# Performance work log

Hardware: AMD Instinct MI355X
Metric: run time of the kernel (lower is better)

## Reference

```python
import jax, jax.numpy as jnp
import numpy as np

N, F, E = 1024, 32, 20


def setup_inputs() -> dict:
    key = jax.random.key(0)
    ks = jax.random.split(key, 18)
    f32 = jnp.float32
    nrm = lambda k, shape, s=1.0: (jax.random.normal(k, shape, f32) * s)
    scalar = nrm(ks[0], (N, 1, F))
    vector = nrm(ks[1], (N, 3, F))
    expansion = nrm(ks[2], (N, N, E))
    d = nrm(ks[3], (N, N, 3))
    direction = d / (jnp.linalg.norm(d, axis=-1, keepdims=True) + 1e-6)
    mask = (jax.random.uniform(ks[4], (N, N, 1)) < 0.9).astype(f32)
    w = 0.1  # weight scale
    return {
        "scalar": scalar, "vector": vector, "expansion": expansion,
        "direction": direction, "mask": mask,
        # message.msg_left: Linear(F,F) -> SiLU -> Linear(F,3F)
        "mL_w1": nrm(ks[5], (F, F), w), "mL_b1": jnp.zeros((F,), f32),
        "mL_w2": nrm(ks[6], (F, 3 * F), w), "mL_b2": jnp.zeros((3 * F,), f32),
        # message.msg_right: Linear(E, 3F)
        "mR_w": nrm(ks[7], (E, 3 * F), w), "mR_b": jnp.zeros((3 * F,), f32),
        # update.upd_right: Linear(2F,F) -> SiLU -> Linear(F,3F)
        "uR_w1": nrm(ks[8], (2 * F, F), w), "uR_b1": jnp.zeros((F,), f32),
        "uR_w2": nrm(ks[9], (F, 3 * F), w), "uR_b2": jnp.zeros((3 * F,), f32),
        # update.U / update.V: Linear(F,F,bias=False)
        "U_w": nrm(ks[10], (F, F), w),
        "V_w": nrm(ks[11], (F, F), w),
    }


def _message(s, v, expansion, direction, mask,
             mL_w1, mL_b1, mL_w2, mL_b2, mR_w, mR_b):
    # msg_left(s): [N,1,F] -> [N,1,3F]
    left = jax.nn.silu(s @ mL_w1 + mL_b1) @ mL_w2 + mL_b2
    # msg_right(expansion): [N,N,E] -> [N,N,3F] -> [N,N,1,3F]
    right = (expansion @ mR_w + mR_b)[..., None, :]
    prod = left * right                      # [N,N,1,3F]
    a, b, c = jnp.split(prod, 3, axis=-1)    # each [N,N,1,F]
    mask_ = mask[..., None]                  # [N,N,1,1]
    delta_s = jnp.sum(mask_ * b, axis=-3)    # [N,1,F]
    dv = v * a + direction[..., None] * c    # [N,N,3,F]
    delta_v = jnp.sum(mask_ * dv, axis=-3)   # [N,3,F]
    return delta_s, delta_v


def _update(scalar, vector, uR_w1, uR_b1, uR_w2, uR_b2, U_w, V_w):
    left = vector @ U_w                      # [N,3,F]
    right = vector @ V_w                     # [N,3,F]
    right_norm = jnp.linalg.norm(right, axis=-2, keepdims=True)   # [N,1,F]
    feats = jnp.concatenate((scalar, right_norm), axis=-1)        # [N,1,2F]
    feats = jax.nn.silu(feats @ uR_w1 + uR_b1) @ uR_w2 + uR_b2    # [N,1,3F]
    a, b, c = jnp.split(feats, 3, axis=-1)
    delta_v = a * left                                            # [N,3,F]
    inner = jnp.sum(left * right, axis=-2, keepdims=True)         # [N,1,F]
    delta_s = inner * b + c
    return delta_s, delta_v


def reference(scalar, vector, expansion, direction, mask,
              mL_w1, mL_b1, mL_w2, mL_b2, mR_w, mR_b,
              uR_w1, uR_b1, uR_w2, uR_b2, U_w, V_w):
    ds, dv = _message(scalar, vector, expansion, direction, mask,
                      mL_w1, mL_b1, mL_w2, mL_b2, mR_w, mR_b)
    scalar = scalar + ds
    vector = vector + dv
    ds, dv = _update(scalar, vector, uR_w1, uR_b1, uR_w2, uR_b2, U_w, V_w)
    return scalar + ds, vector + dv
```

## Files before the change

### kernel.cpp

```cpp
#include <hip/hip_runtime.h>
#include <hip/hip_bf16.h>
#include <math.h>

#define NN 1024

typedef __attribute__((ext_vector_type(8))) short v8s;
typedef __attribute__((ext_vector_type(4))) float v4f;

#define MFMA(a, b, c) __builtin_amdgcn_mfma_f32_16x16x32_bf16((a), (b), (c), 0, 0, 0)

static __device__ __forceinline__ float silu_f(float x) {
    return x / (1.0f + __expf(-x));
}
static __device__ __forceinline__ unsigned short f2bf(float x) {
    __hip_bfloat16 h = __float2bfloat16(x);
    unsigned short u; __builtin_memcpy(&u, &h, 2); return u;
}
static __device__ __forceinline__ unsigned pack2bf(float lo, float hi) {
    __hip_bfloat162 h = __float22bfloat162_rn(make_float2(lo, hi));
    unsigned u; __builtin_memcpy(&u, &h, 4); return u;
}

extern "C" __global__ __launch_bounds__(128)
void node_kernel(const float* __restrict__ scalar,
                 const float* __restrict__ vector,
                 const float* __restrict__ mL_w1, const float* __restrict__ mL_b1,
                 const float* __restrict__ mL_w2, const float* __restrict__ mL_b2,
                 unsigned short* __restrict__ RT)
{
    const int j = blockIdx.x;
    const int t = threadIdx.x;
    __shared__ float ss[32], sh[32], sleft[96];

    if (t < 32) ss[t] = scalar[j * 32 + t];
    __syncthreads();
    if (t < 32) {
        float a = mL_b1[t];
        #pragma unroll
        for (int k = 0; k < 32; k++) a = fmaf(ss[k], mL_w1[k * 32 + t], a);
        sh[t] = silu_f(a);
    }
    __syncthreads();
    if (t < 96) {
        float a = mL_b2[t];
        #pragma unroll
        for (int k = 0; k < 32; k++) a = fmaf(sh[k], mL_w2[k * 96 + t], a);
        sleft[t] = a;
    }
    __syncthreads();
    for (int n = t; n < 160; n += 128) {
        float val;
        if (n < 32)        val = sleft[32 + n];
        else if (n < 128)  val = vector[j * 96 + (n - 32)] * sleft[(n - 32) & 31];
        else               val = sleft[64 + (n - 128)];
        RT[(size_t)n * NN + j] = f2bf(val);
    }
}

extern "C" __global__ __launch_bounds__(128, 3)
void edge_mfma_kernel(const float* __restrict__ scalar,
                      const float* __restrict__ vector,
                      const float* __restrict__ expansion,
                      const float* __restrict__ direction,
                      const float* __restrict__ mask,
                      const float* __restrict__ mR_w, const float* __restrict__ mR_b,
                      const float* __restrict__ uR_w1, const float* __restrict__ uR_b1,
                      const float* __restrict__ uR_w2, const float* __restrict__ uR_b2,
                      const float* __restrict__ U_w,  const float* __restrict__ V_w,
                      const unsigned short* __restrict__ RT,
                      float* __restrict__ out)
{
    const int i = blockIdx.x;
    const int t = threadIdx.x;
    const int wave = t >> 6;
    const int lane = t & 63;
    const int lrow = lane & 15;
    const int quad = lane >> 4;

    __shared__ __align__(16) char smem[24576];
    unsigned short* L1 = (unsigned short*)smem;
    unsigned short* L2 = L1 + 32 * 72;
    float* T1 = (float*)smem;
    float* T2 = T1 + 32 * 128;
    __shared__ float snew[32], vnew[96], lUs[96], rVs[96], rnorm[32], h2s[32], f2s[96];

    v4f acc[12];
    #pragma unroll
    for (int q = 0; q < 12; ++q) acc[q] = (v4f){0.f, 0.f, 0.f, 0.f};

    const int jp = t >> 2;
    const int g  = t & 3;
    const int jl = jp * 2;

    for (int chunk = 0; chunk < 16; ++chunk) {
        const int j0 = chunk * 64;
        {
            const size_t jg = (size_t)i * NN + j0 + jl;
            const float4* ep = (const float4*)(expansion + jg * 20);
            const float m0 = mask[jg], m1 = mask[jg + 1];
            float w0, w1;
            unsigned short *Lp, *Lx;
            if (g == 0) {
                w0 = m0; w1 = m1;
                Lp = L1; Lx = L1 + 20 * 72;
            } else {
                const int d = g - 1;
                w0 = m0 * direction[jg * 3 + d];
                w1 = m1 * direction[(jg + 1) * 3 + d];
                Lp = L2 + d * 20 * 72; Lx = L2 + (60 + d) * 72;
            }
            #pragma unroll
            for (int q = 0; q < 5; ++q) {
                const float4 a = ep[q];
                const float4 b = ep[5 + q];
                *(unsigned*)(Lp + (4 * q + 0) * 72 + jl) = pack2bf(w0 * a.x, w1 * b.x);
                *(unsigned*)(Lp + (4 * q + 1) * 72 + jl) = pack2bf(w0 * a.y, w1 * b.y);
                *(unsigned*)(Lp + (4 * q + 2) * 72 + jl) = pack2bf(w0 * a.z, w1 * b.z);
                *(unsigned*)(Lp + (4 * q + 3) * 72 + jl) = pack2bf(w0 * a.w, w1 * b.w);
            }
            *(unsigned*)(Lx + jl) = pack2bf(w0, w1);
        }
        __syncthreads();
        #pragma unroll
        for (int s = 0; s < 2; ++s) {
            const int koff = s * 32 + quad * 8;
            const v8s a0 = *(const v8s*)(L1 + (lrow) * 72 + koff);
            const v8s a1 = *(const v8s*)(L1 + (16 + lrow) * 72 + koff);
            const unsigned short* Bp = RT + (size_t)lrow * NN + j0 + koff;
            if (wave == 0) {
                #pragma unroll
                for (int nt = 0; nt < 6; ++nt) {
                    const v8s b = *(const v8s*)(Bp + (size_t)nt * 16 * NN);
                    acc[nt]     = MFMA(a0, b, acc[nt]);
                    acc[6 + nt] = MFMA(a1, b, acc[6 + nt]);
                }
            } else {
                const v8s b6 = *(const v8s*)(Bp + (size_t)6 * 16 * NN);
                const v8s b7 = *(const v8s*)(Bp + (size_t)7 * 16 * NN);
                acc[0] = MFMA(a0, b6, acc[0]);
                acc[1] = MFMA(a0, b7, acc[1]);
                acc[2] = MFMA(a1, b6, acc[2]);
                acc[3] = MFMA(a1, b7, acc[3]);
                const v8s d0 = *(const v8s*)(Bp + (size_t)8 * 16 * NN);
                const v8s d1 = *(const v8s*)(Bp + (size_t)9 * 16 * NN);
                #pragma unroll
                for (int mt = 0; mt < 4; ++mt) {
                    const v8s c = *(const v8s*)(L2 + (mt * 16 + lrow) * 72 + koff);
                    acc[4 + mt * 2]     = MFMA(c, d0, acc[4 + mt * 2]);
                    acc[4 + mt * 2 + 1] = MFMA(c, d1, acc[4 + mt * 2 + 1]);
                }
            }
        }
        __syncthreads();
    }

    if (wave == 0) {
        #pragma unroll
        for (int mt = 0; mt < 2; ++mt)
        #pragma unroll
        for (int nt = 0; nt < 6; ++nt) {
            const v4f a = acc[mt * 6 + nt];
            #pragma unroll
            for (int r = 0; r < 4; ++r)
                T1[(mt * 16 + quad * 4 + r) * 128 + nt * 16 + lrow] = a[r];
        }
    } else {
        #pragma unroll
        for (int mt = 0; mt < 2; ++mt)
        #pragma unroll
        for (int nb = 0; nb < 2; ++nb) {
            const v4f a = acc[mt * 2 + nb];
            #pragma unroll
            for (int r = 0; r < 4; ++r)
                T1[(mt * 16 + quad * 4 + r) * 128 + (6 + nb) * 16 + lrow] = a[r];
        }
        #pragma unroll
        for (int mt = 0; mt < 4; ++mt)
        #pragma unroll
        for (int nb = 0; nb < 2; ++nb) {
            const v4f a = acc[4 + mt * 2 + nb];
            #pragma unroll
            for (int r = 0; r < 4; ++r)
                T2[(mt * 16 + quad * 4 + r) * 32 + nb * 16 + lrow] = a[r];
        }
    }
    __syncthreads();

    if (t < 32) {
        const int f = t;
        float a = mR_b[32 + f] * T1[20 * 128 + f];
        #pragma unroll
        for (int e = 0; e < 20; ++e) a = fmaf(mR_w[e * 96 + 32 + f], T1[e * 128 + f], a);
        snew[f] = scalar[i * 32 + f] + a;
    } else if (t < 128) {
        const int q = t - 32, d = q >> 5, f = q & 31;
        const int col = 32 + q;
        float a = mR_b[f] * T1[20 * 128 + col];
        #pragma unroll
        for (int e = 0; e < 20; ++e) a = fmaf(mR_w[e * 96 + f], T1[e * 128 + col], a);
        float c = mR_b[64 + f] * T2[(60 + d) * 32 + f];
        #pragma unroll
        for (int e = 0; e < 20; ++e) c = fmaf(mR_w[e * 96 + 64 + f], T2[(d * 20 + e) * 32 + f], c);
        vnew[q] = vector[i * 96 + q] + a + c;
    }
    __syncthreads();

    if (t < 96) {
        const int d = t >> 5, f = t & 31;
        float au = 0.f, av = 0.f;
        #pragma unroll
        for (int k = 0; k < 32; ++k) {
            const float vv = vnew[d * 32 + k];
            au = fmaf(vv, U_w[k * 32 + f], au);
            av = fmaf(vv, V_w[k * 32 + f], av);
        }
        lUs[t] = au; rVs[t] = av;
    }
    __syncthreads();
    if (t < 32)
        rnorm[t] = sqrtf(rVs[t] * rVs[t] + rVs[32 + t] * rVs[32 + t] + rVs[64 + t] * rVs[64 + t]);
    __syncthreads();
    if (t < 32) {
        float a = uR_b1[t];
        #pragma unroll
        for (int k = 0; k < 32; ++k) a = fmaf(snew[k], uR_w1[k * 32 + t], a);
        #pragma unroll
        for (int k = 0; k < 32; ++k) a = fmaf(rnorm[k], uR_w1[(32 + k) * 32 + t], a);
        h2s[t] = silu_f(a);
    }
    __syncthreads();
    if (t < 96) {
        float a = uR_b2[t];
        #pragma unroll
        for (int k = 0; k < 32; ++k) a = fmaf(h2s[k], uR_w2[k * 96 + t], a);
        f2s[t] = a;
    }
    __syncthreads();
    if (t < 32) {
        const float inner = lUs[t] * rVs[t] + lUs[32 + t] * rVs[32 + t] + lUs[64 + t] * rVs[64 + t];
        out[i * 32 + t] = snew[t] + inner * f2s[32 + t] + f2s[64 + t];
    }
    if (t < 96) {
        out[32768 + i * 96 + t] = vnew[t] + f2s[t & 31] * lUs[t];
    }
}

extern "C" void kernel_launch(void* const* d_in, const int* in_sizes, int n_in,
                              void* d_out, int out_size, void* d_ws, size_t ws_size,
                              hipStream_t stream) {
    const float* scalar    = (const float*)d_in[0];
    const float* vector    = (const float*)d_in[1];
    const float* expansion = (const float*)d_in[2];
    const float* direction = (const float*)d_in[3];
    const float* mask      = (const float*)d_in[4];
    const float* mL_w1     = (const float*)d_in[5];
    const float* mL_b1     = (const float*)d_in[6];
    const float* mL_w2     = (const float*)d_in[7];
    const float* mL_b2     = (const float*)d_in[8];
    const float* mR_w      = (const float*)d_in[9];
    const float* mR_b      = (const float*)d_in[10];
    const float* uR_w1     = (const float*)d_in[11];
    const float* uR_b1     = (const float*)d_in[12];
    const float* uR_w2     = (const float*)d_in[13];
    const float* uR_b2     = (const float*)d_in[14];
    const float* U_w       = (const float*)d_in[15];
    const float* V_w       = (const float*)d_in[16];
    float* out = (float*)d_out;
    unsigned short* RT = (unsigned short*)d_ws;

    hipLaunchKernelGGL(node_kernel, dim3(NN), dim3(128), 0, stream,
                       scalar, vector, mL_w1, mL_b1, mL_w2, mL_b2, RT);
    hipLaunchKernelGGL(edge_mfma_kernel, dim3(NN), dim3(128), 0, stream,
                       scalar, vector, expansion, direction, mask,
                       mR_w, mR_b, uR_w1, uR_b1, uR_w2, uR_b2, U_w, V_w,
                       RT, out);
}
```

Before: 222.5 us.

## Give each wave private staging buffers and drop per-chunk block barriers

The two waves now stage their own operand tiles independently. Wave 0 builds the mask-weighted expansion tile and wave 1 builds the direction-weighted tiles, and each consumes only its own LDS region. This removes the two __syncthreads per chunk and rebalances the MFMA work so wave 0 handles all eight B column tiles. The chunk width drops to 32 columns with a smaller LDS pitch. Each wave now reloads expansion itself, so global traffic grows somewhat, and intra-wave LDS ordering is relied on without explicit barriers.

After: 229.8 us. 1.03x slower.

```diff
diff --git a/kernel.cpp b/kernel.cpp
--- a/kernel.cpp
+++ b/kernel.cpp
@@ -3,6 +3,9 @@
 #include <math.h>
 
 #define NN 1024
+#define KJ 32
+#define NCHUNK (NN / KJ)
+#define LP 40
 
 typedef __attribute__((ext_vector_type(8))) short v8s;
 typedef __attribute__((ext_vector_type(4))) float v4f;
@@ -76,131 +79,149 @@
     const int lane = t & 63;
     const int lrow = lane & 15;
     const int quad = lane >> 4;
-
-    __shared__ __align__(16) char smem[24576];
+    const int jp = lane >> 2;
+    const int g  = lane & 3;
+    const int jl = jp * 2;
+
+    __shared__ __align__(16) char smem[18944];
     unsigned short* L1 = (unsigned short*)smem;
-    unsigned short* L2 = L1 + 32 * 72;
-    float* T1 = (float*)smem;
-    float* T2 = T1 + 32 * 128;
+    unsigned short* L2 = (unsigned short*)(smem + 2560);
+    float* T1c = (float*)smem;
+    float* T2c = (float*)(smem + 10752);
     __shared__ float snew[32], vnew[96], lUs[96], rVs[96], rnorm[32], h2s[32], f2s[96];
 
-    v4f acc[12];
+    v4f acc[16];
     #pragma unroll
-    for (int q = 0; q < 12; ++q) acc[q] = (v4f){0.f, 0.f, 0.f, 0.f};
-
-    const int jp = t >> 2;
-    const int g  = t & 3;
-    const int jl = jp * 2;
-
-    for (int chunk = 0; chunk < 16; ++chunk) {
-        const int j0 = chunk * 64;
-        {
+    for (int q = 0; q < 16; ++q) acc[q] = (v4f){0.f, 0.f, 0.f, 0.f};
+
+    if (wave == 0) {
+        for (int ch = 0; ch < NCHUNK; ++ch) {
+            const int j0 = ch * KJ;
             const size_t jg = (size_t)i * NN + j0 + jl;
-            const float4* ep = (const float4*)(expansion + jg * 20);
+            const float4 fa = *(const float4*)(expansion + jg * 20 + 4 * g);
+            const float4 fb = *(const float4*)(expansion + (jg + 1) * 20 + 4 * g);
             const float m0 = mask[jg], m1 = mask[jg + 1];
-            float w0, w1;
-            unsigned short *Lp, *Lx;
-            if (g == 0) {
-                w0 = m0; w1 = m1;
-                Lp = L1; Lx = L1 + 20 * 72;
+            {
+                const float ea[4] = {fa.x, fa.y, fa.z, fa.w};
+                const float eb[4] = {fb.x, fb.y, fb.z, fb.w};
+                #pragma unroll
+                for (int k = 0; k < 4; ++k)
+                    *(unsigned*)(L1 + (4 * g + k) * LP + jl) = pack2bf(m0 * ea[k], m1 * eb[k]);
+            }
+            if (g == 3) {
+                const float4 ca = *(const float4*)(expansion + jg * 20 + 16);
+                const float4 cb = *(const float4*)(expansion + (jg + 1) * 20 + 16);
+                const float ea[4] = {ca.x, ca.y, ca.z, ca.w};
+                const float eb[4] = {cb.x, cb.y, cb.z, cb.w};
+                #pragma unroll
+                for (int k = 0; k < 4; ++k)
+                    *(unsigned*)(L1 + (16 + k) * LP + jl) = pack2bf(m0 * ea[k], m1 * eb[k]);
+            }
+            if (g == 0) *(unsigned*)(L1 + 20 * LP + jl) = pack2bf(m0, m1);
+
+            const int koff = quad * 8;
+            const v8s a0 = *(const v8s*)(L1 + lrow * LP + koff);
+            const v8s a1 = *(const v8s*)(L1 + (16 + lrow) * LP + koff);
+            const unsigned short* Bp = RT + (size_t)lrow * NN + j0 + koff;
+            #pragma unroll
+            for (int nt = 0; nt < 8; ++nt) {
+                const v8s b = *(const v8s*)(Bp + (size_t)nt * 16 * NN);
+                acc[nt]     = MFMA(a0, b, acc[nt]);
+                acc[8 + nt] = MFMA(a1, b, acc[8 + nt]);
+            }
+        }
+    } else {
+        for (int ch = 0; ch < NCHUNK; ++ch) {
+            const int j0 = ch * KJ;
+            const size_t jg = (size_t)i * NN + j0 + jl;
+            const float m0 = mask[jg], m1 = mask[jg + 1];
+            const float pa[3] = {m0 * direction[jg * 3 + 0],
+                                 m0 * direction[jg * 3 + 1],
+                                 m0 * direction[jg * 3 + 2]};
+            const float pb[3] = {m1 * direction[(jg + 1) * 3 + 0],
+                                 m1 * direction[(jg + 1) * 3 + 1],
+                                 m1 * direction[(jg + 1) * 3 + 2]};
+            const float4 fa = *(const float4*)(expansion + jg * 20 + 4 * g);
+            const float4 fb = *(const float4*)(expansion + (jg + 1) * 20 + 4 * g);
+            const float ea[4] = {fa.x, fa.y, fa.z, fa.w};
+            const float eb[4] = {fb.x, fb.y, fb.z, fb.w};
+            #pragma unroll
+            for (int d = 0; d < 3; ++d)
+                #pragma unroll
+                for (int k = 0; k < 4; ++k)
+                    *(unsigned*)(L2 + (d * 20 + 4 * g + k) * LP + jl) =
+                        pack2bf(pa[d] * ea[k], pb[d] * eb[k]);
+            if (g < 3) {
+                const float4 ca = *(const float4*)(expansion + jg * 20 + 16);
+                const float4 cb = *(const float4*)(expansion + (jg + 1) * 20 + 16);
+                const float sa = (g == 0) ? pa[0] : ((g == 1) ? pa[1] : pa[2]);
+                const float sb = (g == 0) ? pb[0] : ((g == 1) ? pb[1] : pb[2]);
+                const float ea4[4] = {ca.x, ca.y, ca.z, ca.w};
+                const float eb4[4] = {cb.x, cb.y, cb.z, cb.w};
+                #pragma unroll
+                for (int k = 0; k < 4; ++k)
+                    *(unsigned*)(L2 + (g * 20 + 16 + k) * LP + jl) =
+                        pack2bf(sa * ea4[k], sb * eb4[k]);
             } else {
-                const int d = g - 1;
-                w0 = m0 * direction[jg * 3 + d];
-                w1 = m1 * direction[(jg + 1) * 3 + d];
-                Lp = L2 + d * 20 * 72; Lx = L2 + (60 + d) * 72;
-            }
-            #pragma unroll
-            for (int q = 0; q < 5; ++q) {
-                const float4 a = ep[q];
-                const float4 b = ep[5 + q];
-                *(unsigned*)(Lp + (4 * q + 0) * 72 + jl) = pack2bf(w0 * a.x, w1 * b.x);
-                *(unsigned*)(Lp + (4 * q + 1) * 72 + jl) = pack2bf(w0 * a.y, w1 * b.y);
-                *(unsigned*)(Lp + (4 * q + 2) * 72 + jl) = pack2bf(w0 * a.z, w1 * b.z);
-                *(unsigned*)(Lp + (4 * q + 3) * 72 + jl) = pack2bf(w0 * a.w, w1 * b.w);
-            }
-            *(unsigned*)(Lx + jl) = pack2bf(w0, w1);
-        }
-        __syncthreads();
-        #pragma unroll
-        for (int s = 0; s < 2; ++s) {
-            const int koff = s * 32 + quad * 8;
-            const v8s a0 = *(const v8s*)(L1 + (lrow) * 72 + koff);
-            const v8s a1 = *(const v8s*)(L1 + (16 + lrow) * 72 + koff);
-            const unsigned short* Bp = RT + (size_t)lrow * NN + j0 + koff;
-            if (wave == 0) {
-                #pragma unroll
-                for (int nt = 0; nt < 6; ++nt) {
-                    const v8s b = *(const v8s*)(Bp + (size_t)nt * 16 * NN);
-                    acc[nt]     = MFMA(a0, b, acc[nt]);
-                    acc[6 + nt] = MFMA(a1, b, acc[6 + nt]);
-                }
-            } else {
-                const v8s b6 = *(const v8s*)(Bp + (size_t)6 * 16 * NN);
-                const v8s b7 = *(const v8s*)(Bp + (size_t)7 * 16 * NN);
-                acc[0] = MFMA(a0, b6, acc[0]);
-                acc[1] = MFMA(a0, b7, acc[1]);
-                acc[2] = MFMA(a1, b6, acc[2]);
-                acc[3] = MFMA(a1, b7, acc[3]);
-                const v8s d0 = *(const v8s*)(Bp + (size_t)8 * 16 * NN);
-                const v8s d1 = *(const v8s*)(Bp + (size_t)9 * 16 * NN);
-                #pragma unroll
-                for (int mt = 0; mt < 4; ++mt) {
-                    const v8s c = *(const v8s*)(L2 + (mt * 16 + lrow) * 72 + koff);
-                    acc[4 + mt * 2]     = MFMA(c, d0, acc[4 + mt * 2]);
-                    acc[4 + mt * 2 + 1] = MFMA(c, d1, acc[4 + mt * 2 + 1]);
-                }
-            }
-        }
-        __syncthreads();
-    }
-
+                #pragma unroll
+                for (int d = 0; d < 3; ++d)
+                    *(unsigned*)(L2 + (60 + d) * LP + jl) = pack2bf(pa[d], pb[d]);
+            }
+
+            const int koff = quad * 8;
+            const v8s c0 = *(const v8s*)(L2 + (lrow) * LP + koff);
+            const v8s c1 = *(const v8s*)(L2 + (16 + lrow) * LP + koff);
+            const v8s c2 = *(const v8s*)(L2 + (32 + lrow) * LP + koff);
+            const v8s c3 = *(const v8s*)(L2 + (48 + lrow) * LP + koff);
+            const unsigned short* Bp = RT + (size_t)(128 + lrow) * NN + j0 + koff;
+            const v8s b0 = *(const v8s*)(Bp);
+            const v8s b1 = *(const v8s*)(Bp + (size_t)16 * NN);
+            acc[0] = MFMA(c0, b0, acc[0]); acc[1] = MFMA(c0, b1, acc[1]);
+            acc[2] = MFMA(c1, b0, acc[2]); acc[3] = MFMA(c1, b1, acc[3]);
+            acc[4] = MFMA(c2, b0, acc[4]); acc[5] = MFMA(c2, b1, acc[5]);
+            acc[6] = MFMA(c3, b0, acc[6]); acc[7] = MFMA(c3, b1, acc[7]);
+        }
+    }
+
+    __syncthreads();
     if (wave == 0) {
         #pragma unroll
         for (int mt = 0; mt < 2; ++mt)
         #pragma unroll
-        for (int nt = 0; nt < 6; ++nt) {
-            const v4f a = acc[mt * 6 + nt];
-            #pragma unroll
-            for (int r = 0; r < 4; ++r)
-                T1[(mt * 16 + quad * 4 + r) * 128 + nt * 16 + lrow] = a[r];
+        for (int nt = 0; nt < 8; ++nt)
+        #pragma unroll
+        for (int r = 0; r < 4; ++r) {
+            const int row = mt * 16 + quad * 4 + r;
+            if (row <= 20) T1c[row * 128 + nt * 16 + lrow] = acc[mt * 8 + nt][r];
         }
     } else {
         #pragma unroll
-        for (int mt = 0; mt < 2; ++mt)
-        #pragma unroll
-        for (int nb = 0; nb < 2; ++nb) {
-            const v4f a = acc[mt * 2 + nb];
-            #pragma unroll
-            for (int r = 0; r < 4; ++r)
-                T1[(mt * 16 + quad * 4 + r) * 128 + (6 + nb) * 16 + lrow] = a[r];
-        }
-        #pragma unroll
         for (int mt = 0; mt < 4; ++mt)
         #pragma unroll
-        for (int nb = 0; nb < 2; ++nb) {
-            const v4f a = acc[4 + mt * 2 + nb];
-            #pragma unroll
-            for (int r = 0; r < 4; ++r)
-                T2[(mt * 16 + quad * 4 + r) * 32 + nb * 16 + lrow] = a[r];
+        for (int nb = 0; nb < 2; ++nb)
+        #pragma unroll
+        for (int r = 0; r < 4; ++r) {
+            const int row = mt * 16 + quad * 4 + r;
+            if (row <= 62) T2c[row * 32 + nb * 16 + lrow] = acc[mt * 2 + nb][r];
         }
     }
     __syncthreads();
 
     if (t < 32) {
         const int f = t;
-        float a = mR_b[32 + f] * T1[20 * 128 + f];
-        #pragma unroll
-        for (int e = 0; e < 20; ++e) a = fmaf(mR_w[e * 96 + 32 + f], T1[e * 128 + f], a);
+        float a = mR_b[32 + f] * T1c[20 * 128 + f];
+        #pragma unroll
+        for (int e = 0; e < 20; ++e) a = fmaf(mR_w[e * 96 + 32 + f], T1c[e * 128 + f], a);
         snew[f] = scalar[i * 32 + f] + a;
     } else if (t < 128) {
         const int q = t - 32, d = q >> 5, f = q & 31;
         const int col = 32 + q;
-        float a = mR_b[f] * T1[20 * 128 + col];
-        #pragma unroll
-        for (int e = 0; e < 20; ++e) a = fmaf(mR_w[e * 96 + f], T1[e * 128 + col], a);
-        float c = mR_b[64 + f] * T2[(60 + d) * 32 + f];
-        #pragma unroll
-        for (int e = 0; e < 20; ++e) c = fmaf(mR_w[e * 96 + 64 + f], T2[(d * 20 + e) * 32 + f], c);
+        float a = mR_b[f] * T1c[20 * 128 + col];
+        #pragma unroll
+        for (int e = 0; e < 20; ++e) a = fmaf(mR_w[e * 96 + f], T1c[e * 128 + col], a);
+        float c = mR_b[64 + f] * T2c[(60 + d) * 32 + f];
+        #pragma unroll
+        for (int e = 0; e < 20; ++e) c = fmaf(mR_w[e * 96 + 64 + f], T2c[(d * 20 + e) * 32 + f], c);
         vnew[q] = vector[i * 96 + q] + a + c;
     }
     __syncthreads();
```
